# Optimization experiments

Hardware: AMD Instinct MI355X
Metric: run time of the kernel (lower is better)

The kernel has to match this reference:

```python
import jax, jax.numpy as jnp
import numpy as np

B, C, H, W = 16, 256, 56, 56
G, K, R = 16, 3, 2
CR = C // R          # reduced channels = 128
KKG = K * K * G      # span output channels = 144
EPS = 1e-5


def setup_inputs() -> dict:
    key = jax.random.key(0)
    ks = jax.random.split(key, 5)
    return {
        "x": jax.random.normal(ks[0], (B, C, H, W), jnp.float32),
        "w_reduce": jax.random.normal(ks[1], (CR, C), jnp.float32) * 0.05,
        "b_reduce": jax.random.normal(ks[2], (CR,), jnp.float32) * 0.05,
        "gamma": jnp.ones((CR,), jnp.float32),
        "beta": jnp.zeros((CR,), jnp.float32),
        "w_span": jax.random.normal(ks[3], (KKG, CR), jnp.float32) * 0.05,
        "b_span": jax.random.normal(ks[4], (KKG,), jnp.float32) * 0.05,
    }


def _conv1x1(x, w, bias):
    # 1x1 conv == channel contraction
    return jnp.einsum('bchw,oc->bohw', x, w) + bias[None, :, None, None]


def _involution(x, w_reduce, b_reduce, gamma, beta, w_span, b_span):
    b, c, h, w = x.shape
    # kernel-generation branch: reduce -> BN (batch stats) -> ReLU -> span
    t = _conv1x1(x, w_reduce, b_reduce)
    mu = t.mean(axis=(0, 2, 3), keepdims=True)
    var = t.var(axis=(0, 2, 3), keepdims=True)  # biased, as torch BN training
    t = (t - mu) * jax.lax.rsqrt(var + EPS)
    t = t * gamma[None, :, None, None] + beta[None, :, None, None]
    t = jax.nn.relu(t)
    kern = _conv1x1(t, w_span, b_span)  # [b, k*k*g, h, w]
    # 'b (k j g) h w -> b g (k j) h w'
    kern = kern.reshape(b, K, K, G, h, w).transpose(0, 3, 1, 2, 4, 5)
    kern = kern.reshape(b, G, K * K, h, w)
    # unfold x into [b, g, d, k*k, h, w] via shifted padded slices (no dense im2col buffer write pattern beyond necessity)
    p = K // 2
    xp = jnp.pad(x, ((0, 0), (0, 0), (p, p), (p, p)))
    patches = jnp.stack(
        [xp[:, :, i:i + h, j:j + w] for i in range(K) for j in range(K)],
        axis=2)  # [b, c, k*k, h, w]
    patches = patches.reshape(b, G, c // G, K * K, h, w)
    out = jnp.einsum('bgdxhw,bgxhw->bgdhw', patches, kern)  # weighted window sum
    return out.reshape(b, c, h, w)


def reference(x, w_reduce, b_reduce, gamma, beta, w_span, b_span):
    return _involution(x, w_reduce, b_reduce, gamma, beta, w_span, b_span)
```

## Files before the change

kernel.cpp:

```cpp
#include <hip/hip_runtime.h>

#define B_   16
#define C_   256
#define HW_  3136
#define W_   56
#define CR_  128
#define KKG_ 144
#define G_   16
#define NPOS (B_*HW_)
#define EPS_ 1e-5f
#define NBLK 784

typedef float f32x4 __attribute__((ext_vector_type(4)));
typedef short s16x8 __attribute__((ext_vector_type(8)));
typedef short s16x4 __attribute__((ext_vector_type(4)));

#define T2_OFF_B    0
#define KERN_OFF_B  12845056
#define GP_OFF_B    27295744
#define STAT_OFF_B  28098560
#define WBFR_OFF_B  28099584
#define WBFS_OFF_B  28165120

__device__ inline unsigned short f2bf(float f) {
    unsigned u = __float_as_uint(f);
    u += 0x7fff + ((u >> 16) & 1);
    return (unsigned short)(u >> 16);
}
__device__ inline float bf2f(unsigned short h) {
    return __uint_as_float(((unsigned)h) << 16);
}

__global__ __launch_bounds__(256) void prep_cast(
    const float* __restrict__ w_reduce, const float* __restrict__ w_span,
    unsigned short* __restrict__ wbfr, unsigned short* __restrict__ wbfs)
{
    int idx = blockIdx.x * 256 + threadIdx.x;
    if (idx < 32768) {
        wbfr[idx] = f2bf(w_reduce[idx]);
    } else {
        int k = idx - 32768;
        if (k < 18432) wbfs[k] = f2bf(w_span[k]);
    }
}

__global__ __launch_bounds__(256) void reduce_mfma(
    const float* __restrict__ x, const unsigned short* __restrict__ wbfr,
    unsigned short* __restrict__ t2, float* __restrict__ gp)
{
    __shared__ __align__(16) short as_[128 * 40];
    __shared__ __align__(16) short bs_[64 * 40];
    __shared__ float redp[128][2], redq[128][2];

    const int tid = threadIdx.x;
    const int lane = tid & 63, wv = tid >> 6;
    const int q = lane >> 4, i = lane & 15;
    const int mrow = (wv >> 1) * 64, nrow = (wv & 1) * 32;
    const int blk = blockIdx.x;
    const int b = blk / 49;
    const int p0 = (blk % 49) * 64;

    const float* xb = x + (size_t)b * C_ * HW_ + p0;

    const int o_a = tid >> 1, half = tid & 1;
    const int cp = tid >> 4, rq = tid & 15;

    f32x4 acc[4][2] = {};

    for (int c0 = 0; c0 < C_; c0 += 32) {
        {
            const unsigned short* src = wbfr + o_a * C_ + c0 + half * 16;
            s16x8 w0 = *(const s16x8*)src;
            s16x8 w1 = *(const s16x8*)(src + 8);
            *(s16x8*)&as_[o_a * 40 + half * 16] = w0;
            *(s16x8*)&as_[o_a * 40 + half * 16 + 8] = w1;
        }
        {
            const float* s0 = xb + (size_t)(c0 + 2 * cp) * HW_ + rq * 4;
            float4 va = *(const float4*)s0;
            float4 vb = *(const float4*)(s0 + HW_);
            float a4[4] = {va.x, va.y, va.z, va.w};
            float b4[4] = {vb.x, vb.y, vb.z, vb.w};
            #pragma unroll
            for (int j = 0; j < 4; j++) {
                unsigned pk = (unsigned)f2bf(a4[j]) | ((unsigned)f2bf(b4[j]) << 16);
                *(unsigned*)&bs_[(rq * 4 + j) * 40 + 2 * cp] = pk;
            }
        }
        __syncthreads();
        s16x8 af[4], bfr[2];
        #pragma unroll
        for (int mt = 0; mt < 4; mt++)
            af[mt] = *(const s16x8*)&as_[(mrow + mt * 16 + i) * 40 + q * 8];
        #pragma unroll
        for (int nt = 0; nt < 2; nt++)
            bfr[nt] = *(const s16x8*)&bs_[(nrow + nt * 16 + i) * 40 + q * 8];
        #pragma unroll
        for (int mt = 0; mt < 4; mt++)
            #pragma unroll
            for (int nt = 0; nt < 2; nt++)
                acc[mt][nt] = __builtin_amdgcn_mfma_f32_16x16x32_bf16(
                    af[mt], bfr[nt], acc[mt][nt], 0, 0, 0);
        __syncthreads();
    }

    #pragma unroll
    for (int mt = 0; mt < 4; mt++) {
        #pragma unroll
        for (int nt = 0; nt < 2; nt++) {
            #pragma unroll
            for (int reg = 0; reg < 4; reg++) {
                int o = mrow + mt * 16 + q * 4 + reg;
                int p = p0 + nrow + nt * 16 + i;
                t2[((size_t)o * B_ + b) * HW_ + p] = f2bf(acc[mt][nt][reg]);
            }
        }
        #pragma unroll
        for (int reg = 0; reg < 4; reg++) {
            float v0 = acc[mt][0][reg], v1 = acc[mt][1][reg];
            float s = v0 + v1;
            float ss = v0 * v0 + v1 * v1;
            #pragma unroll
            for (int m = 1; m < 16; m <<= 1) {
                s  += __shfl_xor(s, m);
                ss += __shfl_xor(ss, m);
            }
            if (i == 0) {
                int o = mrow + mt * 16 + q * 4 + reg;
                redp[o][wv & 1] = s;
                redq[o][wv & 1] = ss;
            }
        }
    }
    __syncthreads();
    if (tid < 128)
        gp[(size_t)blk * 256 + tid] = redp[tid][0] + redp[tid][1];
    else
        gp[(size_t)blk * 256 + tid] = redq[tid - 128][0] + redq[tid - 128][1];
}

__global__ __launch_bounds__(256) void bn_finalize(
    const float* __restrict__ gp, const float* __restrict__ gamma,
    const float* __restrict__ beta, float* __restrict__ stats)
{
    const int o = blockIdx.x;
    const int tid = threadIdx.x;
    float s = 0.f, ss = 0.f;
    for (int blk = tid; blk < NBLK; blk += 256) {
        s  += gp[(size_t)blk * 256 + o];
        ss += gp[(size_t)blk * 256 + 128 + o];
    }
    #pragma unroll
    for (int m = 1; m < 64; m <<= 1) {
        s  += __shfl_xor(s, m);
        ss += __shfl_xor(ss, m);
    }
    __shared__ float rs[4], rss[4];
    if ((tid & 63) == 0) { rs[tid >> 6] = s; rss[tid >> 6] = ss; }
    __syncthreads();
    if (tid == 0) {
        s  = rs[0] + rs[1] + rs[2] + rs[3];
        ss = rss[0] + rss[1] + rss[2] + rss[3];
        float inv_n = 1.0f / (float)NPOS;
        float mu = s * inv_n;
        float var = ss * inv_n - mu * mu;
        float sc = gamma[o] * rsqrtf(var + EPS_);
        stats[o] = sc;
        stats[128 + o] = beta[o] - mu * sc;
    }
}

__global__ __launch_bounds__(256) void span_mfma(
    const unsigned short* __restrict__ t2, const unsigned short* __restrict__ wbfs,
    const float* __restrict__ b_span, const float* __restrict__ stats,
    unsigned short* __restrict__ kern)
{
    __shared__ __align__(16) short as_[144 * 40];
    __shared__ __align__(16) short bs_[64 * 40];
    __shared__ float scs[128], shs[128], bsp[144];

    const int tid = threadIdx.x;
    const int lane = tid & 63, wv = tid >> 6;
    const int q = lane >> 4, i = lane & 15;
    const int blk = blockIdx.x;
    const int b = blk / 49;
    const int p0 = (blk % 49) * 64;

    if (tid < 128) { scs[tid] = stats[tid]; shs[tid] = stats[128 + tid]; }
    if (tid < 144) bsp[tid] = b_span[tid];
    __syncthreads();

    const int op = tid >> 4, seg = tid & 15;

    f32x4 acc[9] = {};

    for (int c0 = 0; c0 < CR_; c0 += 32) {
        #pragma unroll
        for (int P = 0; P < 3; P++) {
            int idx = P * 256 + tid;
            if (idx < 576) {
                int row = idx >> 2, k8 = idx & 3;
                *(s16x8*)&as_[row * 40 + k8 * 8] =
                    *(const s16x8*)&wbfs[row * CR_ + c0 + k8 * 8];
            }
        }
        {
            int cA = c0 + 2 * op;
            const unsigned short* tA = t2 + ((size_t)cA * B_ + b) * HW_ + p0 + seg * 4;
            s16x4 vA = *(const s16x4*)tA;
            s16x4 vB = *(const s16x4*)(tA + (size_t)B_ * HW_);
            float sA = scs[cA], hA = shs[cA];
            float sB = scs[cA + 1], hB = shs[cA + 1];
            #pragma unroll
            for (int j = 0; j < 4; j++) {
                float fa = fmaxf(fmaf(bf2f((unsigned short)vA[j]), sA, hA), 0.0f);
                float fb = fmaxf(fmaf(bf2f((unsigned short)vB[j]), sB, hB), 0.0f);
                unsigned pk = (unsigned)f2bf(fa) | ((unsigned)f2bf(fb) << 16);
                *(unsigned*)&bs_[(seg * 4 + j) * 40 + 2 * op] = pk;
            }
        }
        __syncthreads();
        s16x8 bfrag = *(const s16x8*)&bs_[(wv * 16 + i) * 40 + q * 8];
        #pragma unroll
        for (int mt = 0; mt < 9; mt++) {
            s16x8 af = *(const s16x8*)&as_[(mt * 16 + i) * 40 + q * 8];
            acc[mt] = __builtin_amdgcn_mfma_f32_16x16x32_bf16(af, bfrag, acc[mt], 0, 0, 0);
        }
        __syncthreads();
    }

    const int p = p0 + wv * 16 + i;
    #pragma unroll
    for (int mt = 0; mt < 9; mt++) {
        #pragma unroll
        for (int reg = 0; reg < 4; reg++) {
            int o2 = mt * 16 + q * 4 + reg;
            kern[((size_t)b * KKG_ + o2) * HW_ + p] = f2bf(acc[mt][reg] + bsp[o2]);
        }
    }
}

__global__ __launch_bounds__(256) void involution_apply(
    const float* __restrict__ x, const unsigned short* __restrict__ kern,
    float* __restrict__ out)
{
    int gtid = blockIdx.x * 256 + threadIdx.x;
    int pix = gtid % HW_;
    int bg  = gtid / HW_;
    int g = bg & 15;
    int b = bg >> 4;
    int h = pix / W_;
    int w = pix % W_;

    const unsigned short* kb = kern + (size_t)b * KKG_ * HW_ + pix;
    float kv[9];
    #pragma unroll
    for (int kk = 0; kk < 9; kk++)
        kv[kk] = bf2f(kb[(size_t)(kk * G_ + g) * HW_]);

    float acc[16];
    #pragma unroll
    for (int d = 0; d < 16; d++) acc[d] = 0.0f;

    const float* xb = x + (size_t)(b * C_ + g * 16) * HW_;
    #pragma unroll
    for (int di = 0; di < 3; di++) {
        int hh = h + di - 1;
        if (hh < 0 || hh >= W_) continue;
        #pragma unroll
        for (int dj = 0; dj < 3; dj++) {
            int ww = w + dj - 1;
            if (ww < 0 || ww >= W_) continue;
            float kval = kv[di * 3 + dj];
            int off = hh * W_ + ww;
            #pragma unroll
            for (int d = 0; d < 16; d++)
                acc[d] = fmaf(xb[(size_t)d * HW_ + off], kval, acc[d]);
        }
    }
    float* ob = out + (size_t)(b * C_ + g * 16) * HW_ + pix;
    #pragma unroll
    for (int d = 0; d < 16; d++) ob[(size_t)d * HW_] = acc[d];
}

extern "C" void kernel_launch(void* const* d_in, const int* in_sizes, int n_in,
                              void* d_out, int out_size, void* d_ws, size_t ws_size,
                              hipStream_t stream) {
    const float* x        = (const float*)d_in[0];
    const float* w_reduce = (const float*)d_in[1];
    const float* gamma    = (const float*)d_in[3];
    const float* beta     = (const float*)d_in[4];
    const float* w_span   = (const float*)d_in[5];
    const float* b_span   = (const float*)d_in[6];
    float* out = (float*)d_out;

    char* wsb = (char*)d_ws;
    unsigned short* t2   = (unsigned short*)(wsb + T2_OFF_B);
    unsigned short* kern = (unsigned short*)(wsb + KERN_OFF_B);
    float*          gp    = (float*)(wsb + GP_OFF_B);
    float*          stats = (float*)(wsb + STAT_OFF_B);
    unsigned short* wbfr = (unsigned short*)(wsb + WBFR_OFF_B);
    unsigned short* wbfs = (unsigned short*)(wsb + WBFS_OFF_B);

    prep_cast<<<200, 256, 0, stream>>>(w_reduce, w_span, wbfr, wbfs);
    reduce_mfma<<<NBLK, 256, 0, stream>>>(x, wbfr, t2, gp);
    bn_finalize<<<128, 256, 0, stream>>>(gp, gamma, beta, stats);
    span_mfma<<<NBLK, 256, 0, stream>>>(t2, wbfs, b_span, stats, kern);
    involution_apply<<<(B_ * G_ * HW_) / 256, 256, 0, stream>>>(x, kern, out);
}
```

Before: 160.5 us.

## Fuse span GEMM with involution apply and pre-swizzle weights into MFMA fragment order

The span 1x1 GEMM and the involution weighted-window sum now run in one kernel. The generated kernels stay in LDS per 64-pixel tile and are never written to or re-read from global memory. Both weight matrices are pre-swizzled into MFMA fragment order, so the GEMMs load A fragments straight from global memory with no LDS staging. The reduce output is now stored pixel-major through an LDS transpose so span can read contiguous rows. The apply stage computes 4 pixels per thread with float4 row loads, which adds register and LDS pressure and may leave edge-halo loads less coalesced.

```diff
diff --git a/kernel.cpp b/kernel.cpp
--- a/kernel.cpp
+++ b/kernel.cpp
@@ -15,12 +15,11 @@
 typedef short s16x8 __attribute__((ext_vector_type(8)));
 typedef short s16x4 __attribute__((ext_vector_type(4)));
 
-#define T2_OFF_B    0
-#define KERN_OFF_B  12845056
-#define GP_OFF_B    27295744
-#define STAT_OFF_B  28098560
-#define WBFR_OFF_B  28099584
-#define WBFS_OFF_B  28165120
+#define TG_OFF_B    0
+#define GP_OFF_B    12845056
+#define STAT_OFF_B  13647872
+#define WBFR_OFF_B  13648896
+#define WBFS_OFF_B  13714432
 
 __device__ inline unsigned short f2bf(float f) {
     unsigned u = __float_as_uint(f);
@@ -33,65 +32,63 @@
 
 __global__ __launch_bounds__(256) void prep_cast(
     const float* __restrict__ w_reduce, const float* __restrict__ w_span,
-    unsigned short* __restrict__ wbfr, unsigned short* __restrict__ wbfs)
+    unsigned short* __restrict__ wbfr_sw, unsigned short* __restrict__ wbfs_sw)
 {
     int idx = blockIdx.x * 256 + threadIdx.x;
     if (idx < 32768) {
-        wbfr[idx] = f2bf(w_reduce[idx]);
+        int row = idx >> 8, col = idx & 255;
+        int k = col >> 5, qq = (col >> 3) & 3, e = col & 7;
+        int half = row >> 6, mt = (row >> 4) & 3, ii = row & 15;
+        int lane = qq * 16 + ii;
+        wbfr_sw[((((k * 2 + half) * 4 + mt) * 64) + lane) * 8 + e] = f2bf(w_reduce[idx]);
     } else {
-        int k = idx - 32768;
-        if (k < 18432) wbfs[k] = f2bf(w_span[k]);
-    }
-}
-
-__global__ __launch_bounds__(256) void reduce_mfma(
-    const float* __restrict__ x, const unsigned short* __restrict__ wbfr,
-    unsigned short* __restrict__ t2, float* __restrict__ gp)
-{
-    __shared__ __align__(16) short as_[128 * 40];
+        int s2 = idx - 32768;
+        int row = s2 >> 7, col = s2 & 127;
+        int k = col >> 5, qq = (col >> 3) & 3, e = col & 7;
+        int mt = row >> 4, ii = row & 15;
+        int lane = qq * 16 + ii;
+        wbfs_sw[(((k * 9 + mt) * 64) + lane) * 8 + e] = f2bf(w_span[s2]);
+    }
+}
+
+__global__ __launch_bounds__(256, 2) void reduce_mfma(
+    const float* __restrict__ x, const unsigned short* __restrict__ wbfr_sw,
+    unsigned short* __restrict__ t_g, float* __restrict__ gp)
+{
     __shared__ __align__(16) short bs_[64 * 40];
-    __shared__ float redp[128][2], redq[128][2];
+    __shared__ __align__(16) short t_tile[64 * 130];
+    __shared__ float redp[256], redq[256];
 
     const int tid = threadIdx.x;
     const int lane = tid & 63, wv = tid >> 6;
     const int q = lane >> 4, i = lane & 15;
-    const int mrow = (wv >> 1) * 64, nrow = (wv & 1) * 32;
+    const int half = wv >> 1, mrow = half * 64, nrow = (wv & 1) * 32;
     const int blk = blockIdx.x;
     const int b = blk / 49;
     const int p0 = (blk % 49) * 64;
 
     const float* xb = x + (size_t)b * C_ * HW_ + p0;
-
-    const int o_a = tid >> 1, half = tid & 1;
     const int cp = tid >> 4, rq = tid & 15;
 
     f32x4 acc[4][2] = {};
 
-    for (int c0 = 0; c0 < C_; c0 += 32) {
-        {
-            const unsigned short* src = wbfr + o_a * C_ + c0 + half * 16;
-            s16x8 w0 = *(const s16x8*)src;
-            s16x8 w1 = *(const s16x8*)(src + 8);
-            *(s16x8*)&as_[o_a * 40 + half * 16] = w0;
-            *(s16x8*)&as_[o_a * 40 + half * 16 + 8] = w1;
-        }
-        {
-            const float* s0 = xb + (size_t)(c0 + 2 * cp) * HW_ + rq * 4;
-            float4 va = *(const float4*)s0;
-            float4 vb = *(const float4*)(s0 + HW_);
-            float a4[4] = {va.x, va.y, va.z, va.w};
-            float b4[4] = {vb.x, vb.y, vb.z, vb.w};
-            #pragma unroll
-            for (int j = 0; j < 4; j++) {
-                unsigned pk = (unsigned)f2bf(a4[j]) | ((unsigned)f2bf(b4[j]) << 16);
-                *(unsigned*)&bs_[(rq * 4 + j) * 40 + 2 * cp] = pk;
-            }
+    for (int k = 0; k < 8; k++) {
+        s16x8 af[4];
+        #pragma unroll
+        for (int mt = 0; mt < 4; mt++)
+            af[mt] = *(const s16x8*)&wbfr_sw[((((k * 2 + half) * 4 + mt) * 64) + lane) * 8];
+        const float* s0 = xb + (size_t)(k * 32 + 2 * cp) * HW_ + rq * 4;
+        float4 va = *(const float4*)s0;
+        float4 vb = *(const float4*)(s0 + HW_);
+        float a4[4] = {va.x, va.y, va.z, va.w};
+        float b4[4] = {vb.x, vb.y, vb.z, vb.w};
+        #pragma unroll
+        for (int j = 0; j < 4; j++) {
+            unsigned pk = (unsigned)f2bf(a4[j]) | ((unsigned)f2bf(b4[j]) << 16);
+            *(unsigned*)&bs_[(rq * 4 + j) * 40 + 2 * cp] = pk;
         }
         __syncthreads();
-        s16x8 af[4], bfr[2];
-        #pragma unroll
-        for (int mt = 0; mt < 4; mt++)
-            af[mt] = *(const s16x8*)&as_[(mrow + mt * 16 + i) * 40 + q * 8];
+        s16x8 bfr[2];
         #pragma unroll
         for (int nt = 0; nt < 2; nt++)
             bfr[nt] = *(const s16x8*)&bs_[(nrow + nt * 16 + i) * 40 + q * 8];
@@ -108,18 +105,15 @@
     for (int mt = 0; mt < 4; mt++) {
         #pragma unroll
         for (int nt = 0; nt < 2; nt++) {
-            #pragma unroll
-            for (int reg = 0; reg < 4; reg++) {
-                int o = mrow + mt * 16 + q * 4 + reg;
-                int p = p0 + nrow + nt * 16 + i;
-                t2[((size_t)o * B_ + b) * HW_ + p] = f2bf(acc[mt][nt][reg]);
-            }
+            s16x4 hv;
+            #pragma unroll
+            for (int reg = 0; reg < 4; reg++) hv[reg] = (short)f2bf(acc[mt][nt][reg]);
+            *(s16x4*)&t_tile[(nrow + nt * 16 + i) * 130 + mrow + mt * 16 + q * 4] = hv;
         }
         #pragma unroll
         for (int reg = 0; reg < 4; reg++) {
             float v0 = acc[mt][0][reg], v1 = acc[mt][1][reg];
-            float s = v0 + v1;
-            float ss = v0 * v0 + v1 * v1;
+            float s = v0 + v1, ss = v0 * v0 + v1 * v1;
             #pragma unroll
             for (int m = 1; m < 16; m <<= 1) {
                 s  += __shfl_xor(s, m);
@@ -127,16 +121,26 @@
             }
             if (i == 0) {
                 int o = mrow + mt * 16 + q * 4 + reg;
-                redp[o][wv & 1] = s;
-                redq[o][wv & 1] = ss;
+                redp[o * 2 + (wv & 1)] = s;
+                redq[o * 2 + (wv & 1)] = ss;
             }
         }
     }
     __syncthreads();
     if (tid < 128)
-        gp[(size_t)blk * 256 + tid] = redp[tid][0] + redp[tid][1];
+        gp[(size_t)blk * 256 + tid] = redp[tid * 2] + redp[tid * 2 + 1];
     else
-        gp[(size_t)blk * 256 + tid] = redq[tid - 128][0] + redq[tid - 128][1];
+        gp[(size_t)blk * 256 + tid] = redq[(tid - 128) * 2] + redq[(tid - 128) * 2 + 1];
+
+    {
+        const int p = tid >> 2, part = tid & 3;
+        const short* src = &t_tile[p * 130 + part * 32];
+        unsigned short* dst = t_g + ((size_t)blk * 64 + p) * 128 + part * 32;
+        *(s16x8*)(dst)      = *(const s16x8*)(src);
+        *(s16x8*)(dst + 8)  = *(const s16x8*)(src + 8);
+        *(s16x8*)(dst + 16) = *(const s16x8*)(src + 16);
+        *(s16x8*)(dst + 24) = *(const s16x8*)(src + 24);
+    }
 }
 
 __global__ __launch_bounds__(256) void bn_finalize(
@@ -170,13 +174,12 @@
     }
 }
 
-__global__ __launch_bounds__(256) void span_mfma(
-    const unsigned short* __restrict__ t2, const unsigned short* __restrict__ wbfs,
-    const float* __restrict__ b_span, const float* __restrict__ stats,
-    unsigned short* __restrict__ kern)
-{
-    __shared__ __align__(16) short as_[144 * 40];
-    __shared__ __align__(16) short bs_[64 * 40];
+__global__ __launch_bounds__(256, 2) void span_invol(
+    const float* __restrict__ x, const unsigned short* __restrict__ t_g,
+    const unsigned short* __restrict__ wbfs_sw, const float* __restrict__ b_span,
+    const float* __restrict__ stats, float* __restrict__ out)
+{
+    __shared__ __align__(16) short kt[64 * 152];
     __shared__ float scs[128], shs[128], bsp[144];
 
     const int tid = threadIdx.x;
@@ -190,97 +193,82 @@
     if (tid < 144) bsp[tid] = b_span[tid];
     __syncthreads();
 
-    const int op = tid >> 4, seg = tid & 15;
-
-    f32x4 acc[9] = {};
-
-    for (int c0 = 0; c0 < CR_; c0 += 32) {
-        #pragma unroll
-        for (int P = 0; P < 3; P++) {
-            int idx = P * 256 + tid;
-            if (idx < 576) {
-                int row = idx >> 2, k8 = idx & 3;
-                *(s16x8*)&as_[row * 40 + k8 * 8] =
-                    *(const s16x8*)&wbfs[row * CR_ + c0 + k8 * 8];
-            }
-        }
-        {
-            int cA = c0 + 2 * op;
-            const unsigned short* tA = t2 + ((size_t)cA * B_ + b) * HW_ + p0 + seg * 4;
-            s16x4 vA = *(const s16x4*)tA;
-            s16x4 vB = *(const s16x4*)(tA + (size_t)B_ * HW_);
-            float sA = scs[cA], hA = shs[cA];
-            float sB = scs[cA + 1], hB = shs[cA + 1];
-            #pragma unroll
-            for (int j = 0; j < 4; j++) {
-                float fa = fmaxf(fmaf(bf2f((unsigned short)vA[j]), sA, hA), 0.0f);
-                float fb = fmaxf(fmaf(bf2f((unsigned short)vB[j]), sB, hB), 0.0f);
-                unsigned pk = (unsigned)f2bf(fa) | ((unsigned)f2bf(fb) << 16);
-                *(unsigned*)&bs_[(seg * 4 + j) * 40 + 2 * op] = pk;
-            }
-        }
-        __syncthreads();
-        s16x8 bfrag = *(const s16x8*)&bs_[(wv * 16 + i) * 40 + q * 8];
+    {
+        const int pl = wv * 16 + i;
+        const unsigned short* trow = t_g + ((size_t)blk * 64 + pl) * 128;
+        f32x4 acc[9] = {};
+        for (int k = 0; k < 4; k++) {
+            s16x8 raw = *(const s16x8*)&trow[k * 32 + q * 8];
+            float4 sc0 = *(const float4*)&scs[k * 32 + q * 8];
+            float4 sc1 = *(const float4*)&scs[k * 32 + q * 8 + 4];
+            float4 sh0 = *(const float4*)&shs[k * 32 + q * 8];
+            float4 sh1 = *(const float4*)&shs[k * 32 + q * 8 + 4];
+            float scv[8] = {sc0.x, sc0.y, sc0.z, sc0.w, sc1.x, sc1.y, sc1.z, sc1.w};
+            float shv[8] = {sh0.x, sh0.y, sh0.z, sh0.w, sh1.x, sh1.y, sh1.z, sh1.w};
+            s16x8 bfrag;
+            #pragma unroll
+            for (int j = 0; j < 8; j++) {
+                float f = fmaxf(fmaf(bf2f((unsigned short)raw[j]), scv[j], shv[j]), 0.0f);
+                bfrag[j] = (short)f2bf(f);
+            }
+            #pragma unroll
+            for (int mt = 0; mt < 9; mt++) {
+                s16x8 af = *(const s16x8*)&wbfs_sw[(((k * 9 + mt) * 64) + lane) * 8];
+                acc[mt] = __builtin_amdgcn_mfma_f32_16x16x32_bf16(af, bfrag, acc[mt], 0, 0, 0);
+            }
+        }
         #pragma unroll
         for (int mt = 0; mt < 9; mt++) {
-            s16x8 af = *(const s16x8*)&as_[(mt * 16 + i) * 40 + q * 8];
-            acc[mt] = __builtin_amdgcn_mfma_f32_16x16x32_bf16(af, bfrag, acc[mt], 0, 0, 0);
-        }
-        __syncthreads();
-    }
-
-    const int p = p0 + wv * 16 + i;
-    #pragma unroll
-    for (int mt = 0; mt < 9; mt++) {
-        #pragma unroll
-        for (int reg = 0; reg < 4; reg++) {
-            int o2 = mt * 16 + q * 4 + reg;
-            kern[((size_t)b * KKG_ + o2) * HW_ + p] = f2bf(acc[mt][reg] + bsp[o2]);
-        }
-    }
-}
-
-__global__ __launch_bounds__(256) void involution_apply(
-    const float* __restrict__ x, const unsigned short* __restrict__ kern,
-    float* __restrict__ out)
-{
-    int gtid = blockIdx.x * 256 + threadIdx.x;
-    int pix = gtid % HW_;
-    int bg  = gtid / HW_;
-    int g = bg & 15;
-    int b = bg >> 4;
-    int h = pix / W_;
-    int w = pix % W_;
-
-    const unsigned short* kb = kern + (size_t)b * KKG_ * HW_ + pix;
-    float kv[9];
-    #pragma unroll
-    for (int kk = 0; kk < 9; kk++)
-        kv[kk] = bf2f(kb[(size_t)(kk * G_ + g) * HW_]);
-
-    float acc[16];
-    #pragma unroll
-    for (int d = 0; d < 16; d++) acc[d] = 0.0f;
-
-    const float* xb = x + (size_t)(b * C_ + g * 16) * HW_;
-    #pragma unroll
-    for (int di = 0; di < 3; di++) {
-        int hh = h + di - 1;
-        if (hh < 0 || hh >= W_) continue;
-        #pragma unroll
-        for (int dj = 0; dj < 3; dj++) {
-            int ww = w + dj - 1;
-            if (ww < 0 || ww >= W_) continue;
-            float kval = kv[di * 3 + dj];
-            int off = hh * W_ + ww;
-            #pragma unroll
-            for (int d = 0; d < 16; d++)
-                acc[d] = fmaf(xb[(size_t)d * HW_ + off], kval, acc[d]);
-        }
-    }
-    float* ob = out + (size_t)(b * C_ + g * 16) * HW_ + pix;
-    #pragma unroll
-    for (int d = 0; d < 16; d++) ob[(size_t)d * HW_] = acc[d];
+            s16x4 hv;
+            #pragma unroll
+            for (int reg = 0; reg < 4; reg++)
+                hv[reg] = (short)f2bf(acc[mt][reg] + bsp[mt * 16 + q * 4 + reg]);
+            *(s16x4*)&kt[pl * 152 + mt * 16 + q * 4] = hv;
+        }
+    }
+    __syncthreads();
+
+    {
+        const int g = tid >> 4, grp = tid & 15;
+        const int pix = p0 + grp * 4;
+        const int h = pix / W_, w0 = pix - h * W_;
+
+        float kv[9][4];
+        #pragma unroll
+        for (int kk = 0; kk < 9; kk++)
+            #pragma unroll
+            for (int j = 0; j < 4; j++)
+                kv[kk][j] = bf2f((unsigned short)kt[(grp * 4 + j) * 152 + kk * 16 + g]);
+
+        const bool wl = (w0 > 0), wr = (w0 < W_ - 4);
+        const float* xb2 = x + (size_t)(b * C_ + g * 16) * HW_;
+        float* ob = out + (size_t)(b * C_ + g * 16) * HW_ + pix;
+
+        #pragma unroll 4
+        for (int d = 0; d < 16; d++) {
+            const float* xd = xb2 + (size_t)d * HW_;
+            float a0 = 0.f, a1 = 0.f, a2 = 0.f, a3 = 0.f;
+            #pragma unroll
+            for (int di = 0; di < 3; di++) {
+                int hh = h + di - 1;
+                if (hh < 0 || hh >= W_) continue;
+                const float* rowp = xd + hh * W_ + w0;
+                float4 m = *(const float4*)rowp;
+                float e0 = wl ? rowp[-1] : 0.f;
+                float e5 = wr ? rowp[4]  : 0.f;
+                float e[6] = {e0, m.x, m.y, m.z, m.w, e5};
+                #pragma unroll
+                for (int dj = 0; dj < 3; dj++) {
+                    const float* kvt = kv[di * 3 + dj];
+                    a0 = fmaf(e[0 + dj], kvt[0], a0);
+                    a1 = fmaf(e[1 + dj], kvt[1], a1);
+                    a2 = fmaf(e[2 + dj], kvt[2], a2);
+                    a3 = fmaf(e[3 + dj], kvt[3], a3);
+                }
+            }
+            *(float4*)(ob + (size_t)d * HW_) = make_float4(a0, a1, a2, a3);
+        }
+    }
 }
 
 extern "C" void kernel_launch(void* const* d_in, const int* in_sizes, int n_in,
@@ -295,16 +283,14 @@
     float* out = (float*)d_out;
 
     char* wsb = (char*)d_ws;
-    unsigned short* t2   = (unsigned short*)(wsb + T2_OFF_B);
-    unsigned short* kern = (unsigned short*)(wsb + KERN_OFF_B);
-    float*          gp    = (float*)(wsb + GP_OFF_B);
-    float*          stats = (float*)(wsb + STAT_OFF_B);
-    unsigned short* wbfr = (unsigned short*)(wsb + WBFR_OFF_B);
-    unsigned short* wbfs = (unsigned short*)(wsb + WBFS_OFF_B);
-
-    prep_cast<<<200, 256, 0, stream>>>(w_reduce, w_span, wbfr, wbfs);
-    reduce_mfma<<<NBLK, 256, 0, stream>>>(x, wbfr, t2, gp);
+    unsigned short* t_g     = (unsigned short*)(wsb + TG_OFF_B);
+    float*          gp      = (float*)(wsb + GP_OFF_B);
+    float*          stats   = (float*)(wsb + STAT_OFF_B);
+    unsigned short* wbfr_sw = (unsigned short*)(wsb + WBFR_OFF_B);
+    unsigned short* wbfs_sw = (unsigned short*)(wsb + WBFS_OFF_B);
+
+    prep_cast<<<200, 256, 0, stream>>>(w_reduce, w_span, wbfr_sw, wbfs_sw);
+    reduce_mfma<<<NBLK, 256, 0, stream>>>(x, wbfr_sw, t_g, gp);
     bn_finalize<<<128, 256, 0, stream>>>(gp, gamma, beta, stats);
-    span_mfma<<<NBLK, 256, 0, stream>>>(t2, wbfs, b_span, stats, kern);
-    involution_apply<<<(B_ * G_ * HW_) / 256, 256, 0, stream>>>(x, kern, out);
-}
+    span_invol<<<NBLK, 256, 0, stream>>>(x, t_g, wbfs_sw, b_span, stats, out);
+}
```

Measured after the change: 167.8 us. 4.6% more time.
